# Kernel tuning notes

Measured on AMD Instinct MI355X. Metric: run time of the kernel, lower is better.

## Reference

```python
import jax, jax.numpy as jnp
import numpy as np

N, L, D = 8192, 50, 64          # batch nodes, history length, embed_dim
NUM_ITEMS, NUM_ATTRS, NUM_FAM = 50000, 100000, 100000


def setup_inputs() -> dict:
    key = jax.random.key(0)
    ks = jax.random.split(key, 12)
    scale = 0.05
    return {
        "nodes": jax.random.randint(ks[0], (N,), 0, NUM_ITEMS),
        "history_va": jax.random.randint(ks[1], (N, L), 0, NUM_ATTRS),
        "history_af": jax.random.randint(ks[2], (N, L), 0, NUM_FAM),
        "v2e_w": jax.random.normal(ks[3], (NUM_ITEMS, D), jnp.float32) * scale,
        "a2e_w": jax.random.normal(ks[4], (NUM_ATTRS, D), jnp.float32) * scale,
        "f2e_w": jax.random.normal(ks[5], (NUM_FAM, D), jnp.float32) * scale,
        "W1": jax.random.normal(ks[6], (3 * D, D), jnp.float32) * scale,
        "b1": jnp.zeros((D,), jnp.float32),
        "W2": jax.random.normal(ks[7], (D, D), jnp.float32) * scale,
        "b2": jnp.zeros((D,), jnp.float32),
        "w3": jax.random.normal(ks[8], (D, 1), jnp.float32) * scale,
        "b3": jnp.zeros((1,), jnp.float32),
    }


def reference(nodes, history_va, history_af, v2e_w, a2e_w, f2e_w,
              W1, b1, W2, b2, w3, b3):
    # Batched form of the per-node loop (va=True branch).
    e_va = a2e_w[history_va]                       # [N, L, D] gathered attr embeds
    e_af = f2e_w[history_af]                       # [N, L, D] gathered famous embeds
    va_rep = v2e_w[nodes]                          # [N, D]    target item embed
    rep = jnp.broadcast_to(va_rep[:, None, :], e_va.shape)
    x = jnp.concatenate([e_va, rep, e_af], axis=-1)  # [N, L, 3D]
    h = jax.nn.relu(x @ W1 + b1)                   # [N, L, D]
    h = jax.nn.relu(h @ W2 + b2)                   # [N, L, D]
    scores = (h @ w3 + b3)[..., 0]                 # [N, L]
    att = jax.nn.softmax(scores, axis=1)           # softmax over history dim
    # e_va.T @ att per node  ==  weighted sum over history
    return jnp.einsum("nld,nl->nd", e_va, att)     # [N, D]
```

## Files before the change

### kernel.cpp

```cpp
#include <hip/hip_runtime.h>
#include <hip/hip_bf16.h>

typedef __bf16    bf16x8 __attribute__((ext_vector_type(8)));
typedef __bf16    bf16x4 __attribute__((ext_vector_type(4)));
typedef _Float16  f16x8  __attribute__((ext_vector_type(8)));
typedef _Float16  f16x4  __attribute__((ext_vector_type(4)));
typedef float     f32x4  __attribute__((ext_vector_type(4)));

#define HL 50
#define DD 64


__global__ __launch_bounds__(256, 4) void prep_all_kernel(
    const int*   __restrict__ nodes,
    const float* __restrict__ v2e,
    const float* __restrict__ a2e,
    const float* __restrict__ f2e,
    const float* __restrict__ W1,
    const float* __restrict__ b1,
    const float* __restrict__ W2,
    const float* __restrict__ b2,
    const float* __restrict__ w3,
    _Float16* __restrict__ A2, _Float16* __restrict__ F2,
    _Float16* __restrict__ E16, _Float16* __restrict__ ba16,
    _Float16* __restrict__ w2f, float* __restrict__ wsc,
    int nA, int nF, int N, int GAF, int GB)
{
    __shared__ __align__(16) _Float16 wlds[8 * 512];
    __shared__ __align__(16) _Float16 es[64 * 72];
    const int tid  = threadIdx.x;
    const int w    = tid >> 6, lane = tid & 63;
    const int lq   = lane & 15, quad = lane >> 4;
    const int bid  = blockIdx.x;

    if (bid < 2 * GAF) {
        const bool  isA   = (bid < GAF);
        const int   t0    = isA ? bid : bid - GAF;
        const int   nrows = isA ? nA : nF;
        const int   NT    = (nrows + 63) >> 6;
        const float* src  = isA ? a2e : f2e;
        const float* Wp   = isA ? W1 : (W1 + 128 * DD);
        _Float16*   dst   = isA ? A2 : F2;
        _Float16*   ws_   = &es[w * 16 * 72];

        auto loadtile = [&](int tb, float4 (&vv)[4], int (&gg)[4]) {
            const int r0w = tb * 64 + w * 16;
            #pragma unroll
            for (int i = 0; i < 4; ++i) {
                int t = i * 64 + lane;
                int row = t >> 4, chunk = t & 15;
                int gr = r0w + row; if (gr >= nrows) gr = nrows - 1;
                gg[i] = gr;
                vv[i] = *(const float4*)(src + (size_t)gr * DD + chunk * 4);
            }
        };

        #pragma unroll
        for (int h = 0; h < 2; ++h) {
            int combo = w + 4 * h;
            int ct = combo >> 1, t = combo & 1;
            f16x8 pk;
            #pragma unroll
            for (int j = 0; j < 8; ++j)
                pk[j] = (_Float16)Wp[(t * 32 + quad * 8 + j) * DD + ct * 16 + lq];
            *(f16x8*)&wlds[(size_t)combo * 512 + lane * 8] = pk;
        }

        int    tb = t0;
        float4 v[4];
        int    grv[4];
        loadtile(tb, v, grv);

        __syncthreads();

        for (;;) {
            const int r0w = tb * 64 + w * 16;

            #pragma unroll
            for (int i = 0; i < 4; ++i) {
                int t = i * 64 + lane;
                int row = t >> 4, chunk = t & 15;
                f16x4 pk = {(_Float16)v[i].x, (_Float16)v[i].y,
                            (_Float16)v[i].z, (_Float16)v[i].w};
                *(f16x4*)&ws_[row * 72 + chunk * 4] = pk;
                if (isA) *(f16x4*)(E16 + (size_t)grv[i] * DD + chunk * 4) = pk;
            }

            const int tn = tb + GAF;
            float4 vn[4];
            int    grn[4];
            if (tn < NT) loadtile(tn, vn, grn);

            f16x8 afr[2];
            #pragma unroll
            for (int t = 0; t < 2; ++t)
                afr[t] = *(const f16x8*)&ws_[lq * 72 + t * 32 + quad * 8];
            f32x4 acc[4];
            #pragma unroll
            for (int ct = 0; ct < 4; ++ct) {
                acc[ct] = (f32x4){0.f, 0.f, 0.f, 0.f};
                #pragma unroll
                for (int t = 0; t < 2; ++t) {
                    f16x8 bfr = *(const f16x8*)&wlds[(size_t)(ct * 2 + t) * 512 + lane * 8];
                    acc[ct] = __builtin_amdgcn_mfma_f32_16x16x32_f16(afr[t], bfr, acc[ct], 0, 0, 0);
                }
            }

            #pragma unroll
            for (int ct = 0; ct < 4; ++ct)
                #pragma unroll
                for (int r = 0; r < 4; ++r)
                    ws_[(quad * 4 + r) * 72 + ct * 16 + lq] = (_Float16)acc[ct][r];
            {
                int row = lane >> 2, g = lane & 3;
                int gr  = r0w + row;
                if (gr < nrows) {
                    f16x8 v0 = *(const f16x8*)&ws_[row * 72 + g * 16];
                    f16x8 v1 = *(const f16x8*)&ws_[row * 72 + g * 16 + 8];
                    *(f16x8*)(dst + (size_t)gr * DD + g * 16)     = v0;
                    *(f16x8*)(dst + (size_t)gr * DD + g * 16 + 8) = v1;
                }
            }

            if (tn >= NT) break;
            tb = tn;
            #pragma unroll
            for (int i = 0; i < 4; ++i) { v[i] = vn[i]; grv[i] = grn[i]; }
        }
    } else if (bid < 2 * GAF + GB) {
        const int col = w * 16 + lq;
        const int n0 = (bid - 2 * GAF) * 64;
        #pragma unroll
        for (int i = 0; i < 4; ++i) {
            int t = i * 256 + tid;
            int row = t >> 4, q = t & 15;
            int gn = n0 + row; if (gn >= N) gn = N - 1;
            int idx = nodes[gn];
            float4 v = *(const float4*)(v2e + (size_t)idx * DD + q * 4);
            f16x4 pk = {(_Float16)v.x, (_Float16)v.y, (_Float16)v.z, (_Float16)v.w};
            *(f16x4*)&es[row * 72 + q * 4] = pk;
        }
        f16x8 bfr[2];
        #pragma unroll
        for (int t = 0; t < 2; ++t)
            #pragma unroll
            for (int j = 0; j < 8; ++j)
                bfr[t][j] = (_Float16)W1[(64 + t * 32 + quad * 8 + j) * DD + col];
        const float b1c = b1[col];
        __syncthreads();

        f32x4 acc[4];
        #pragma unroll
        for (int mt = 0; mt < 4; ++mt) acc[mt] = (f32x4){0.f, 0.f, 0.f, 0.f};
        #pragma unroll
        for (int t = 0; t < 2; ++t)
            #pragma unroll
            for (int mt = 0; mt < 4; ++mt) {
                f16x8 a = *(const f16x8*)&es[(mt * 16 + lq) * 72 + t * 32 + quad * 8];
                acc[mt] = __builtin_amdgcn_mfma_f32_16x16x32_f16(a, bfr[t], acc[mt], 0, 0, 0);
            }
        #pragma unroll
        for (int mt = 0; mt < 4; ++mt)
            #pragma unroll
            for (int r = 0; r < 4; ++r) {
                int gn = n0 + mt * 16 + quad * 4 + r;
                if (gn < N) ba16[(size_t)gn * DD + col] = (_Float16)(acc[mt][r] + b1c);
            }
    } else {
        const int ln = tid & 63, c0 = tid >> 6;
        #pragma unroll
        for (int h = 0; h < 2; ++h) {
            int combo = c0 + 4 * h;
            int ct = combo >> 1, t = combo & 1;
            _Float16* d = w2f + ((size_t)combo * 64 + ln) * 8;
            #pragma unroll
            for (int j = 0; j < 8; ++j)
                d[j] = (_Float16)W2[(t * 32 + (ln >> 4) * 8 + j) * DD + ct * 16 + (ln & 15)];
        }
        if (tid < 64) { wsc[tid] = w3[tid]; wsc[64 + tid] = b2[tid]; }
    }
}

__global__ __launch_bounds__(256, 6) void va_main_kernel(
    const int*      __restrict__ hva,
    const int*      __restrict__ haf,
    const _Float16* __restrict__ A2,
    const _Float16* __restrict__ F2,
    const _Float16* __restrict__ E16,
    const _Float16* __restrict__ ba16,
    const _Float16* __restrict__ w2f,
    const float*    __restrict__ wsc,
    float*          __restrict__ out, int Ntot)
{
    const int tid  = threadIdx.x;
    const int w    = tid >> 6;
    const int lane = tid & 63;
    const int lq   = lane & 15;
    const int quad = lane >> 4;
    const int node = blockIdx.x * 4 + w;
    if (node >= Ntot) return;

    const int* hb = hva + node * HL;
    const int* fb = haf + node * HL;
    const int lclamp = (lane < HL) ? lane : 0;
    const int iv  = hb[lclamp];
    const int ifv = fb[lclamp];

    f16x8 bag[2];
    #pragma unroll
    for (int t = 0; t < 2; ++t)
        bag[t] = *(const f16x8*)(ba16 + (size_t)node * DD + t * 32 + quad * 8);

    f16x8 a2g[4][2], f2g[4][2];
    #pragma unroll
    for (int mt = 0; mt < 4; ++mt) {
        const int row = mt * 16 + lq;
        const int ia  = __shfl(iv,  row);
        const int ifm = __shfl(ifv, row);
        const bool valid = (row < HL);
        #pragma unroll
        for (int t = 0; t < 2; ++t) {
            if (valid) {
                a2g[mt][t] = *(const f16x8*)(A2 + (size_t)ia  * DD + t * 32 + quad * 8);
                f2g[mt][t] = *(const f16x8*)(F2 + (size_t)ifm * DD + t * 32 + quad * 8);
            }
        }
    }

    f16x8 h1f[4][2];
    #pragma unroll
    for (int mt = 0; mt < 4; ++mt) {
        const bool valid = (mt * 16 + lq) < HL;
        #pragma unroll
        for (int t = 0; t < 2; ++t) {
            f16x8 h = a2g[mt][t] + f2g[mt][t] + bag[t];
            #pragma unroll
            for (int j = 0; j < 8; ++j)
                h1f[mt][t][j] = (valid && h[j] > (_Float16)0.f) ? h[j] : (_Float16)0.f;
        }
    }

    float sc[4][4];
    #pragma unroll
    for (int mt = 0; mt < 4; ++mt)
        #pragma unroll
        for (int r = 0; r < 4; ++r) sc[mt][r] = 0.f;

    #pragma unroll
    for (int ct = 0; ct < 4; ++ct) {
        const float b2c = wsc[64 + ct * 16 + lq];
        const float w3c = wsc[ct * 16 + lq];
        f16x8 bfr[2];
        #pragma unroll
        for (int t = 0; t < 2; ++t)
            bfr[t] = *(const f16x8*)(w2f + ((size_t)(ct * 2 + t) * 64 + lane) * 8);
        #pragma unroll
        for (int mt = 0; mt < 4; ++mt) {
            f32x4 acc = {b2c, b2c, b2c, b2c};
            #pragma unroll
            for (int t = 0; t < 2; ++t)
                acc = __builtin_amdgcn_mfma_f32_16x16x32_f16(h1f[mt][t], bfr[t], acc, 0, 0, 0);
            #pragma unroll
            for (int r = 0; r < 4; ++r)
                sc[mt][r] = fmaf(fmaxf(acc[r], 0.f), w3c, sc[mt][r]);
        }
    }

    #pragma unroll
    for (int mt = 0; mt < 4; ++mt)
        #pragma unroll
        for (int r = 0; r < 4; ++r)
            #pragma unroll
            for (int m = 1; m < 16; m <<= 1)
                sc[mt][r] += __shfl_xor(sc[mt][r], m);

    #pragma unroll
    for (int r = 0; r < 4; ++r)
        if (48 + quad * 4 + r >= HL) sc[3][r] = -3.0e38f;

    float mx = sc[0][0];
    #pragma unroll
    for (int mt = 0; mt < 4; ++mt)
        #pragma unroll
        for (int r = 0; r < 4; ++r) mx = fmaxf(mx, sc[mt][r]);
    mx = fmaxf(mx, __shfl_xor(mx, 16));
    mx = fmaxf(mx, __shfl_xor(mx, 32));

    float sm = 0.f;
    #pragma unroll
    for (int mt = 0; mt < 4; ++mt)
        #pragma unroll
        for (int r = 0; r < 4; ++r) {
            sc[mt][r] = __expf(sc[mt][r] - mx);
            sm += sc[mt][r];
        }
    sm += __shfl_xor(sm, 16);
    sm += __shfl_xor(sm, 32);
    const float inv = 1.f / sm;

    float oa[4] = {0.f, 0.f, 0.f, 0.f};
    #pragma unroll
    for (int l = 0; l < HL; ++l) {
        const int   srcl = ((l >> 2) & 3) << 4;
        const float av   = __shfl(sc[l >> 4][l & 3], srcl);
        const int   idx  = __builtin_amdgcn_readlane(iv, l);
        oa[l & 3] = fmaf(av, (float)E16[(size_t)idx * DD + lane], oa[l & 3]);
    }
    out[(size_t)node * DD + lane] = ((oa[0] + oa[1]) + (oa[2] + oa[3])) * inv;
}

#define FMR  112
#define FMT  7
#define FXSS 136

__global__ __launch_bounds__(256) void fb_prep_kernel(
    const float* __restrict__ W1, const float* __restrict__ W2,
    const float* __restrict__ w3, const float* __restrict__ b1,
    const float* __restrict__ b2,
    __bf16* __restrict__ wf, float* __restrict__ wsc)
{
    const int tid  = threadIdx.x;
    const int quad = tid >> 6;
    const int col  = tid & 63;
    __bf16* dst = wf + tid * 64;
    #pragma unroll
    for (int t = 0; t < 4; ++t)
        #pragma unroll
        for (int j = 0; j < 8; ++j) {
            int keff = t * 32 + quad * 8 + j;
            int krow = (keff < 64) ? keff : keff + 64;
            dst[t * 8 + j] = (__bf16)W1[krow * 64 + col];
        }
    #pragma unroll
    for (int t = 0; t < 2; ++t)
        #pragma unroll
        for (int j = 0; j < 8; ++j) {
            dst[32 + t * 8 + j] = (__bf16)W1[(64 + t * 32 + quad * 8 + j) * 64 + col];
            dst[48 + t * 8 + j] = (__bf16)W2[(t * 32 + quad * 8 + j) * 64 + col];
        }
    if (tid < 64) {
        wsc[tid] = w3[tid]; wsc[64 + tid] = b1[tid]; wsc[128 + tid] = b2[tid];
    }
}

__global__ __launch_bounds__(256, 5) void fb_agg_kernel(
    const int* __restrict__ nodes, const int* __restrict__ hva,
    const int* __restrict__ haf, const float* __restrict__ v2e,
    const float* __restrict__ a2e, const float* __restrict__ f2e,
    const __bf16* __restrict__ wf, const float* __restrict__ wsc,
    float* __restrict__ out)
{
    __shared__ __bf16 xs[FMR * FXSS];
    __shared__ float  pbuf[4 * FMR];
    const int tid = threadIdx.x;
    const int w = tid >> 6, lane = tid & 63, lq = lane & 15, quad = lane >> 4;
    const int col = w * 16 + lq;
    const int n0 = blockIdx.x * 2;
    {
        const int* hb = hva + n0 * HL;
        const int* fb = haf + n0 * HL;
        #pragma unroll
        for (int i = 0; i < 13; ++i) {
            int t = i * 256 + tid;
            if (t < 2 * HL * 2 * 16) {
                int r = t >> 4, q = t & 15;
                bool va = (r < 2 * HL);
                int gr = va ? r : r - 2 * HL;
                int idx = va ? hb[gr] : fb[gr];
                const float* src = (va ? a2e : f2e) + (size_t)idx * DD + q * 4;
                float4 v = *(const float4*)src;
                bf16x4 pk = {(__bf16)v.x, (__bf16)v.y, (__bf16)v.z, (__bf16)v.w};
                *(bf16x4*)&xs[gr * FXSS + (va ? 0 : DD) + q * 4] = pk;
            }
        }
    }
    bf16x8 repf[2];
    #pragma unroll
    for (int t = 0; t < 2; ++t)
        #pragma unroll
        for (int j = 0; j < 8; ++j) repf[t][j] = (__bf16)0.f;
    if (lq < 2) {
        int nd = nodes[n0 + lq];
        const float* rp = v2e + (size_t)nd * DD;
        #pragma unroll
        for (int t = 0; t < 2; ++t) {
            float4 v0 = *(const float4*)(rp + t * 32 + quad * 8);
            float4 v1 = *(const float4*)(rp + t * 32 + quad * 8 + 4);
            repf[t] = (bf16x8){(__bf16)v0.x, (__bf16)v0.y, (__bf16)v0.z, (__bf16)v0.w,
                               (__bf16)v1.x, (__bf16)v1.y, (__bf16)v1.z, (__bf16)v1.w};
        }
    }
    const __bf16* fbp = wf + (size_t)(quad * 64 + col) * 64;
    bf16x8 b1f[4], b1u[2], b2f[2];
    #pragma unroll
    for (int t = 0; t < 4; ++t) b1f[t] = *(const bf16x8*)(fbp + t * 8);
    #pragma unroll
    for (int t = 0; t < 2; ++t) {
        b1u[t] = *(const bf16x8*)(fbp + 32 + t * 8);
        b2f[t] = *(const bf16x8*)(fbp + 48 + t * 8);
    }
    const float w3c = wsc[col];
    const float b1c = wsc[64 + col];
    const float b2c = wsc[128 + col];
    f32x4 rb = {0.f, 0.f, 0.f, 0.f};
    #pragma unroll
    for (int t = 0; t < 2; ++t)
        rb = __builtin_amdgcn_mfma_f32_16x16x32_bf16(repf[t], b1u[t], rb, 0, 0, 0);
    const float bias0 = __shfl(rb[0], lq) + b1c;
    const float bias1 = __shfl(rb[1], lq) + b1c;
    __syncthreads();
    f32x4 acc[FMT];
    #pragma unroll
    for (int mt = 0; mt < FMT; ++mt)
        #pragma unroll
        for (int r = 0; r < 4; ++r) {
            int gr = mt * 16 + quad * 4 + r;
            acc[mt][r] = (gr >= HL) ? bias1 : bias0;
        }
    #pragma unroll
    for (int t = 0; t < 4; ++t)
        #pragma unroll
        for (int mt = 0; mt < FMT; ++mt) {
            bf16x8 a = *(const bf16x8*)&xs[(mt * 16 + lq) * FXSS + t * 32 + quad * 8];
            acc[mt] = __builtin_amdgcn_mfma_f32_16x16x32_bf16(a, b1f[t], acc[mt], 0, 0, 0);
        }
    __syncthreads();
    #pragma unroll
    for (int mt = 0; mt < FMT; ++mt)
        #pragma unroll
        for (int r = 0; r < 4; ++r) {
            int gr = mt * 16 + quad * 4 + r;
            xs[gr * FXSS + DD + col] = (__bf16)fmaxf(acc[mt][r], 0.f);
        }
    __syncthreads();
    f32x4 a2[FMT];
    #pragma unroll
    for (int mt = 0; mt < FMT; ++mt) a2[mt] = (f32x4){b2c, b2c, b2c, b2c};
    #pragma unroll
    for (int t = 0; t < 2; ++t)
        #pragma unroll
        for (int mt = 0; mt < FMT; ++mt) {
            bf16x8 a = *(const bf16x8*)&xs[(mt * 16 + lq) * FXSS + DD + t * 32 + quad * 8];
            a2[mt] = __builtin_amdgcn_mfma_f32_16x16x32_bf16(a, b2f[t], a2[mt], 0, 0, 0);
        }
    #pragma unroll
    for (int mt = 0; mt < FMT; ++mt) {
        float p0 = fmaxf(a2[mt][0], 0.f) * w3c;
        float p1 = fmaxf(a2[mt][1], 0.f) * w3c;
        float p2 = fmaxf(a2[mt][2], 0.f) * w3c;
        float p3 = fmaxf(a2[mt][3], 0.f) * w3c;
        #pragma unroll
        for (int m = 1; m < 16; m <<= 1) {
            p0 += __shfl_xor(p0, m); p1 += __shfl_xor(p1, m);
            p2 += __shfl_xor(p2, m); p3 += __shfl_xor(p3, m);
        }
        if (lq == 0) {
            int rowb = mt * 16 + quad * 4;
            pbuf[w * FMR + rowb + 0] = p0; pbuf[w * FMR + rowb + 1] = p1;
            pbuf[w * FMR + rowb + 2] = p2; pbuf[w * FMR + rowb + 3] = p3;
        }
    }
    __syncthreads();
    const int n = w & 1, lh = w >> 1;
    float att;
    {
        float s = -3.0e38f;
        if (lane < HL) {
            int gr = n * HL + lane;
            s = pbuf[gr] + pbuf[FMR + gr] + pbuf[2 * FMR + gr] + pbuf[3 * FMR + gr];
        }
        float mx = s;
        #pragma unroll
        for (int m = 1; m < 64; m <<= 1) mx = fmaxf(mx, __shfl_xor(mx, m));
        float e = (lane < HL) ? __expf(s - mx) : 0.f;
        float sm = e;
        #pragma unroll
        for (int m = 1; m < 64; m <<= 1) sm += __shfl_xor(sm, m);
        att = e / sm;
    }
    {
        float o = 0.f;
        const int lb = lh * 25;
        #pragma unroll
        for (int i = 0; i < 25; ++i) {
            int l = lb + i;
            float av = __shfl(att, l);
            o = fmaf(av, (float)xs[(n * HL + l) * FXSS + lane], o);
        }
        float* op = (float*)&xs[(100 + w) * FXSS + DD];
        op[lane] = o;
    }
    __syncthreads();
    if (w < 2) {
        const float* p0 = (const float*)&xs[(100 + w) * FXSS + DD];
        const float* p1 = (const float*)&xs[(100 + w + 2) * FXSS + DD];
        out[(size_t)(n0 + w) * DD + lane] = p0[lane] + p1[lane];
    }
}

extern "C" void kernel_launch(void* const* d_in, const int* in_sizes, int n_in,
                              void* d_out, int out_size, void* d_ws, size_t ws_size,
                              hipStream_t stream) {
    const int*   nodes = (const int*)d_in[0];
    const int*   hva   = (const int*)d_in[1];
    const int*   haf   = (const int*)d_in[2];
    const float* v2e   = (const float*)d_in[3];
    const float* a2e   = (const float*)d_in[4];
    const float* f2e   = (const float*)d_in[5];
    const float* W1    = (const float*)d_in[6];
    const float* b1    = (const float*)d_in[7];
    const float* W2    = (const float*)d_in[8];
    const float* b2    = (const float*)d_in[9];
    const float* w3    = (const float*)d_in[10];
    float* out = (float*)d_out;

    const int N  = in_sizes[0];
    const int nA = in_sizes[4] / DD;
    const int nF = in_sizes[5] / DD;

    size_t offA2 = 0;
    size_t offF2 = (offA2 + (size_t)nA * DD * 2 + 255) & ~(size_t)255;
    size_t offE  = (offF2 + (size_t)nF * DD * 2 + 255) & ~(size_t)255;
    size_t offBA = (offE  + (size_t)nA * DD * 2 + 255) & ~(size_t)255;
    size_t offWF = (offBA + (size_t)N * DD * 2 + 255) & ~(size_t)255;
    size_t offSC = offWF + 8 * 64 * 8 * 2;
    size_t need  = offSC + 128 * 4;

    if (ws_size >= need) {
        _Float16* A2  = (_Float16*)((char*)d_ws + offA2);
        _Float16* F2  = (_Float16*)((char*)d_ws + offF2);
        _Float16* E16 = (_Float16*)((char*)d_ws + offE);
        _Float16* ba  = (_Float16*)((char*)d_ws + offBA);
        _Float16* w2f = (_Float16*)((char*)d_ws + offWF);
        float*    wsc = (float*)((char*)d_ws + offSC);

        const int GAF = 448;
        const int GB  = (N + 63) / 64;
        prep_all_kernel<<<2 * GAF + GB + 1, 256, 0, stream>>>(
            nodes, v2e, a2e, f2e, W1, b1, W2, b2, w3,
            A2, F2, E16, ba, w2f, wsc, nA, nF, N, GAF, GB);
        va_main_kernel<<<(N + 3) / 4, 256, 0, stream>>>(
            hva, haf, A2, F2, E16, ba, w2f, wsc, out, N);
    } else {
        __bf16* wf  = (__bf16*)d_ws;
        float*  wsc = (float*)((char*)d_ws + 256 * 64 * 2);
        fb_prep_kernel<<<1, 256, 0, stream>>>(W1, W2, w3, b1, b2, wf, wsc);
        fb_agg_kernel<<<N / 2, 256, 0, stream>>>(nodes, hva, haf, v2e, a2e, f2e,
                                                 wf, wsc, out);
    }
}
```

Baseline: 164.4 us.

## Interleave projected and raw attr embeddings in one table, deepen prefetch

Merges the projected attribute table (A2) and the fp16 raw attribute embedding copy (E16) into a single 128-wide interleaved row, so the main kernel's gather for the MLP input and the weighted-sum gather touch the same row and cache lines. The prep loop now keeps two tiles in flight (double-buffered register prefetch two strides ahead), GAF drops from 448 to 320, and va_main's occupancy hint goes from 6 to 4. These changes aim to improve gather locality and hide load latency during preprocessing. The cost is more registers per thread and a wider row stride, which may hurt coalescing of the projected gather.

```diff
diff --git a/kernel.cpp b/kernel.cpp
--- a/kernel.cpp
+++ b/kernel.cpp
@@ -21,8 +21,8 @@
     const float* __restrict__ W2,
     const float* __restrict__ b2,
     const float* __restrict__ w3,
-    _Float16* __restrict__ A2, _Float16* __restrict__ F2,
-    _Float16* __restrict__ E16, _Float16* __restrict__ ba16,
+    _Float16* __restrict__ AE, _Float16* __restrict__ F2,
+    _Float16* __restrict__ ba16,
     _Float16* __restrict__ w2f, float* __restrict__ wsc,
     int nA, int nF, int N, int GAF, int GB)
 {
@@ -34,14 +34,15 @@
     const int bid  = blockIdx.x;
 
     if (bid < 2 * GAF) {
-        const bool  isA   = (bid < GAF);
-        const int   t0    = isA ? bid : bid - GAF;
-        const int   nrows = isA ? nA : nF;
-        const int   NT    = (nrows + 63) >> 6;
-        const float* src  = isA ? a2e : f2e;
-        const float* Wp   = isA ? W1 : (W1 + 128 * DD);
-        _Float16*   dst   = isA ? A2 : F2;
-        _Float16*   ws_   = &es[w * 16 * 72];
+        const bool  isA    = (bid < GAF);
+        const int   t0     = isA ? bid : bid - GAF;
+        const int   nrows  = isA ? nA : nF;
+        const int   NT     = (nrows + 63) >> 6;
+        const int   dstride= isA ? 128 : 64;
+        const float* src   = isA ? a2e : f2e;
+        const float* Wp    = isA ? W1 : (W1 + 128 * DD);
+        _Float16*   dst    = isA ? AE : F2;
+        _Float16*   ws_    = &es[w * 16 * 72];
 
         auto loadtile = [&](int tb, float4 (&vv)[4], int (&gg)[4]) {
             const int r0w = tb * 64 + w * 16;
@@ -55,41 +56,20 @@
             }
         };
 
-        #pragma unroll
-        for (int h = 0; h < 2; ++h) {
-            int combo = w + 4 * h;
-            int ct = combo >> 1, t = combo & 1;
-            f16x8 pk;
-            #pragma unroll
-            for (int j = 0; j < 8; ++j)
-                pk[j] = (_Float16)Wp[(t * 32 + quad * 8 + j) * DD + ct * 16 + lq];
-            *(f16x8*)&wlds[(size_t)combo * 512 + lane * 8] = pk;
-        }
-
-        int    tb = t0;
-        float4 v[4];
-        int    grv[4];
-        loadtile(tb, v, grv);
-
-        __syncthreads();
-
-        for (;;) {
-            const int r0w = tb * 64 + w * 16;
-
+        auto proc = [&](int tbc, float4 (&vv)[4], int (&gg)[4]) {
+            const int r0w = tbc * 64 + w * 16;
             #pragma unroll
             for (int i = 0; i < 4; ++i) {
                 int t = i * 64 + lane;
                 int row = t >> 4, chunk = t & 15;
-                f16x4 pk = {(_Float16)v[i].x, (_Float16)v[i].y,
-                            (_Float16)v[i].z, (_Float16)v[i].w};
+                f16x4 pk = {(_Float16)vv[i].x, (_Float16)vv[i].y,
+                            (_Float16)vv[i].z, (_Float16)vv[i].w};
                 *(f16x4*)&ws_[row * 72 + chunk * 4] = pk;
-                if (isA) *(f16x4*)(E16 + (size_t)grv[i] * DD + chunk * 4) = pk;
-            }
-
-            const int tn = tb + GAF;
-            float4 vn[4];
-            int    grn[4];
-            if (tn < NT) loadtile(tn, vn, grn);
+                if (isA)
+                    *(f16x4*)(dst + (size_t)gg[i] * 128 + 64 + chunk * 4) = pk;
+            }
+            const int tn2 = tbc + 2 * GAF;
+            if (tn2 < NT) loadtile(tn2, vv, gg);
 
             f16x8 afr[2];
             #pragma unroll
@@ -117,15 +97,36 @@
                 if (gr < nrows) {
                     f16x8 v0 = *(const f16x8*)&ws_[row * 72 + g * 16];
                     f16x8 v1 = *(const f16x8*)&ws_[row * 72 + g * 16 + 8];
-                    *(f16x8*)(dst + (size_t)gr * DD + g * 16)     = v0;
-                    *(f16x8*)(dst + (size_t)gr * DD + g * 16 + 8) = v1;
+                    *(f16x8*)(dst + (size_t)gr * dstride + g * 16)     = v0;
+                    *(f16x8*)(dst + (size_t)gr * dstride + g * 16 + 8) = v1;
                 }
             }
-
-            if (tn >= NT) break;
-            tb = tn;
-            #pragma unroll
-            for (int i = 0; i < 4; ++i) { v[i] = vn[i]; grv[i] = grn[i]; }
+        };
+
+        #pragma unroll
+        for (int h = 0; h < 2; ++h) {
+            int combo = w + 4 * h;
+            int ct = combo >> 1, t = combo & 1;
+            f16x8 pk;
+            #pragma unroll
+            for (int j = 0; j < 8; ++j)
+                pk[j] = (_Float16)Wp[(t * 32 + quad * 8 + j) * DD + ct * 16 + lq];
+            *(f16x8*)&wlds[(size_t)combo * 512 + lane * 8] = pk;
+        }
+
+        int    tb = t0;
+        float4 vA[4], vB[4];
+        int    gA[4], gB[4];
+        loadtile(tb, vA, gA);
+        if (tb + GAF < NT) loadtile(tb + GAF, vB, gB);
+
+        __syncthreads();
+
+        for (;;) {
+            proc(tb, vA, gA);
+            tb += GAF; if (tb >= NT) break;
+            proc(tb, vB, gB);
+            tb += GAF; if (tb >= NT) break;
         }
     } else if (bid < 2 * GAF + GB) {
         const int col = w * 16 + lq;
@@ -181,12 +182,11 @@
     }
 }
 
-__global__ __launch_bounds__(256, 6) void va_main_kernel(
+__global__ __launch_bounds__(256, 4) void va_main_kernel(
     const int*      __restrict__ hva,
     const int*      __restrict__ haf,
-    const _Float16* __restrict__ A2,
+    const _Float16* __restrict__ AE,
     const _Float16* __restrict__ F2,
-    const _Float16* __restrict__ E16,
     const _Float16* __restrict__ ba16,
     const _Float16* __restrict__ w2f,
     const float*    __restrict__ wsc,
@@ -221,8 +221,8 @@
         #pragma unroll
         for (int t = 0; t < 2; ++t) {
             if (valid) {
-                a2g[mt][t] = *(const f16x8*)(A2 + (size_t)ia  * DD + t * 32 + quad * 8);
-                f2g[mt][t] = *(const f16x8*)(F2 + (size_t)ifm * DD + t * 32 + quad * 8);
+                a2g[mt][t] = *(const f16x8*)(AE + (size_t)ia  * 128 + t * 32 + quad * 8);
+                f2g[mt][t] = *(const f16x8*)(F2 + (size_t)ifm * DD  + t * 32 + quad * 8);
             }
         }
     }
@@ -304,7 +304,7 @@
         const int   srcl = ((l >> 2) & 3) << 4;
         const float av   = __shfl(sc[l >> 4][l & 3], srcl);
         const int   idx  = __builtin_amdgcn_readlane(iv, l);
-        oa[l & 3] = fmaf(av, (float)E16[(size_t)idx * DD + lane], oa[l & 3]);
+        oa[l & 3] = fmaf(av, (float)AE[(size_t)idx * 128 + 64 + lane], oa[l & 3]);
     }
     out[(size_t)node * DD + lane] = ((oa[0] + oa[1]) + (oa[2] + oa[3])) * inv;
 }
@@ -518,29 +518,27 @@
     const int nA = in_sizes[4] / DD;
     const int nF = in_sizes[5] / DD;
 
-    size_t offA2 = 0;
-    size_t offF2 = (offA2 + (size_t)nA * DD * 2 + 255) & ~(size_t)255;
-    size_t offE  = (offF2 + (size_t)nF * DD * 2 + 255) & ~(size_t)255;
-    size_t offBA = (offE  + (size_t)nA * DD * 2 + 255) & ~(size_t)255;
+    size_t offAE = 0;
+    size_t offF2 = (offAE + (size_t)nA * 128 * 2 + 255) & ~(size_t)255;
+    size_t offBA = (offF2 + (size_t)nF * DD * 2 + 255) & ~(size_t)255;
     size_t offWF = (offBA + (size_t)N * DD * 2 + 255) & ~(size_t)255;
     size_t offSC = offWF + 8 * 64 * 8 * 2;
     size_t need  = offSC + 128 * 4;
 
     if (ws_size >= need) {
-        _Float16* A2  = (_Float16*)((char*)d_ws + offA2);
+        _Float16* AE  = (_Float16*)((char*)d_ws + offAE);
         _Float16* F2  = (_Float16*)((char*)d_ws + offF2);
-        _Float16* E16 = (_Float16*)((char*)d_ws + offE);
         _Float16* ba  = (_Float16*)((char*)d_ws + offBA);
         _Float16* w2f = (_Float16*)((char*)d_ws + offWF);
         float*    wsc = (float*)((char*)d_ws + offSC);
 
-        const int GAF = 448;
+        const int GAF = 320;
         const int GB  = (N + 63) / 64;
         prep_all_kernel<<<2 * GAF + GB + 1, 256, 0, stream>>>(
             nodes, v2e, a2e, f2e, W1, b1, W2, b2, w3,
-            A2, F2, E16, ba, w2f, wsc, nA, nF, N, GAF, GB);
+            AE, F2, ba, w2f, wsc, nA, nF, N, GAF, GB);
         va_main_kernel<<<(N + 3) / 4, 256, 0, stream>>>(
-            hva, haf, A2, F2, E16, ba, w2f, wsc, out, N);
+            hva, haf, AE, F2, ba, w2f, wsc, out, N);
     } else {
         __bf16* wf  = (__bf16*)d_ws;
         float*  wsc = (float*)((char*)d_ws + 256 * 64 * 2);
```

New measurement: 148.0 us. 1.11x faster.
